# Performance work log

Hardware: AMD Instinct MI355X
Metric: run time of the kernel (lower is better)

Reference implementation:

```python
import jax, jax.numpy as jnp
import numpy as np

EPS = 1e-5
N_NODES = 50000


def batchnorm(x, gamma, beta):
    # training-mode BatchNorm1d: batch mean, biased variance
    mean = jnp.mean(x, axis=0)
    var = jnp.mean(jnp.square(x - mean), axis=0)
    return (x - mean) * jax.lax.rsqrt(var + EPS) * gamma + beta


def setup_inputs() -> dict:
    key = jax.random.key(0)
    ks = jax.random.split(key, 8)
    N, E, D_IN, D_H, D_OUT = N_NODES, 800000, 128, 128, 128
    feat = jax.random.normal(ks[0], (N, D_IN), dtype=jnp.float32)
    w = jax.random.uniform(ks[1], (E,), dtype=jnp.float32)
    # xavier_uniform with relu gain for Q and W
    gain = float(np.sqrt(2.0))
    bq = gain * np.sqrt(6.0 / (D_IN + D_H))
    bw = gain * np.sqrt(6.0 / (D_IN + D_H + D_OUT))
    Q_w = jax.random.uniform(ks[2], (D_H, D_IN), minval=-bq, maxval=bq, dtype=jnp.float32)
    W_w = jax.random.uniform(ks[3], (D_OUT, D_IN + D_H), minval=-bw, maxval=bw, dtype=jnp.float32)
    Q_b = jnp.zeros((D_H,), jnp.float32)
    W_b = jnp.zeros((D_OUT,), jnp.float32)
    gamma2 = jnp.ones((D_OUT,), jnp.float32)
    beta2 = jnp.zeros((D_OUT,), jnp.float32)
    src = jax.random.randint(ks[4], (E,), 0, N, dtype=jnp.int32)
    dst = jax.random.randint(ks[5], (E,), 0, N, dtype=jnp.int32)
    return {"feat": feat, "w": w, "Q_w": Q_w, "Q_b": Q_b, "W_w": W_w,
            "W_b": W_b, "gamma2": gamma2, "beta2": beta2, "src": src, "dst": dst}


def reference(feat, w, Q_w, Q_b, W_w, W_b, gamma2, beta2, src, dst):
    N = feat.shape[0]
    # h = dropout(bnorm_two(relu(Q(feat))))  (dropout=0 -> identity; source reuses bnorm_two)
    h = batchnorm(jax.nn.relu(feat @ Q_w.T + Q_b), gamma2, beta2)  # [N, H]
    # weighted neighbor mean: sum_e w_e * h[src_e] scattered to dst, / sum_e w_e
    num = jax.ops.segment_sum(w[:, None] * h[src], dst, num_segments=N)  # [N, H]
    den = jax.ops.segment_sum(w, dst, num_segments=N)  # [N]
    has_msg = den[:, None] != 0
    agg = jnp.where(has_msg, num / jnp.where(has_msg, den[:, None], 1.0), h)
    rst = jnp.concatenate([feat, agg], axis=1) @ W_w.T + W_b  # [N, OUT]
    rst = batchnorm(jax.nn.relu(rst), gamma2, beta2)
    denom = jnp.linalg.norm(rst, axis=1, keepdims=True)
    return rst / jnp.where(denom == 0, 1.0, denom)
```

## Files before the change

kernel.cpp:

```cpp
#include <hip/hip_runtime.h>
#include <stdint.h>


#define BN_EPS 1e-5f
#define NSLOT 32

typedef __attribute__((ext_vector_type(8))) short bf16x8;
typedef __attribute__((ext_vector_type(4))) float f32x4;

static __device__ __forceinline__ unsigned short f2bf(float f) {
    uint32_t u = __builtin_bit_cast(uint32_t, f);
    u += 0x7fffu + ((u >> 16) & 1u);
    return (unsigned short)(u >> 16);
}
static __device__ __forceinline__ float bf_lo(uint32_t u) {
    return __builtin_bit_cast(float, u << 16);
}
static __device__ __forceinline__ float bf_hi(uint32_t u) {
    return __builtin_bit_cast(float, u & 0xffff0000u);
}

static __device__ __forceinline__ void cast_blk(
    const float* __restrict__ src, unsigned short* __restrict__ dst,
    int n, int blk)
{
    int i = (blk * 256 + threadIdx.x) * 4;
    if (i + 3 < n) {
        float4 v = *(const float4*)(src + i);
        ushort4 o;
        o.x = f2bf(v.x); o.y = f2bf(v.y); o.z = f2bf(v.z); o.w = f2bf(v.w);
        *(ushort4*)(dst + i) = o;
    } else {
        for (int j = i; j < n; ++j) dst[j] = f2bf(src[j]);
    }
}

static __device__ __forceinline__ void scan_ccnt(
    const int* __restrict__ ccnt, int* excl_out, int* v_out, int* w0s)
{
    const int t = threadIdx.x;
    int v = 0, incl = 0;
    if (t < 128) {
        v = ccnt[t];
        incl = v;
        const int lane = t & 63;
#pragma unroll
        for (int o = 1; o < 64; o <<= 1) {
            int u = __shfl_up(incl, o, 64);
            if (lane >= o) incl += u;
        }
        if (t == 63) *w0s = incl;
    }
    __syncthreads();
    int excl = 0;
    if (t < 128) excl = incl - v + ((t >> 6) ? *w0s : 0);
    *excl_out = excl;
    *v_out = v;
}

__global__ __launch_bounds__(256) void k_pre(
    const float* __restrict__ feat, unsigned short* __restrict__ featb, int nf,
    const int* __restrict__ dst, int* __restrict__ ccnt, int E, int CB, int HB,
    const float* __restrict__ Qw, unsigned short* __restrict__ Qwb,
    const float* __restrict__ Ww, unsigned short* __restrict__ Wwb,
    int* __restrict__ offs, int N)
{
    int b = (int)blockIdx.x;
    if (b < CB) {
        if (b == 0 && threadIdx.x == 0) offs[N] = E;
        cast_blk(feat, featb, nf, b);
        return;
    }
    b -= CB;
    if (b >= HB) {
        b -= HB;
        if (b < 16) cast_blk(Qw, Qwb, 128 * 128, b);
        else        cast_blk(Ww, Wwb, 128 * 256, b - 16);
        return;
    }
    __shared__ int hcnt[128];
    const int tid = threadIdx.x;
    if (tid < 128) hcnt[tid] = 0;
    __syncthreads();
    const int base_e = b * 2048;
#pragma unroll
    for (int j = 0; j < 8; ++j) {
        int e = base_e + j * 256 + tid;
        if (e < E) atomicAdd(&hcnt[dst[e] >> 9], 1);
    }
    __syncthreads();
    if (tid < 128 && hcnt[tid] > 0) atomicAdd(&ccnt[tid], hcnt[tid]);
}

template<int K, bool OUT_BF16>
static __device__ __forceinline__ void gemm_body(
    int bid,
    const unsigned short* __restrict__ A_lo,
    const unsigned short* __restrict__ A_hi,
    const unsigned short* __restrict__ Bb,
    const float* __restrict__ bias,
    void* __restrict__ Yv,
    double* __restrict__ sum, double* __restrict__ sumsq, int N)
{
    constexpr int SA = 72;
    __shared__ unsigned short As[64 * SA];
    __shared__ unsigned short Bs[128 * SA];
    __shared__ float bsum_s[128], bsq_s[128];

    const int tid  = threadIdx.x;
    const int lane = tid & 63;
    const int wv   = tid >> 6;
    const int wr   = wv >> 1;
    const int wc   = wv & 1;
    const int m15  = lane & 15;
    const int quad = lane >> 4;
    const int r0   = bid * 64;

    if (tid < 128) { bsum_s[tid] = 0.f; bsq_s[tid] = 0.f; }

    f32x4 acc[2][4];
#pragma unroll
    for (int rt = 0; rt < 2; ++rt)
#pragma unroll
        for (int ct = 0; ct < 4; ++ct)
            acc[rt][ct] = (f32x4){0.f, 0.f, 0.f, 0.f};

    for (int kc = 0; kc < K; kc += 64) {
        const unsigned short* Ap = (kc < 128) ? A_lo : A_hi;
        const int koff = kc & 127;
#pragma unroll
        for (int i = 0; i < 2; ++i) {
            int idx = i * 256 + tid;
            int row = idx >> 3, seg = idx & 7;
            int gr  = r0 + row; if (gr >= N) gr = N - 1;
            uint4 v = *(const uint4*)(Ap + (size_t)gr * 128 + koff + seg * 8);
            *(uint4*)(As + row * SA + seg * 8) = v;
        }
#pragma unroll
        for (int i = 0; i < 4; ++i) {
            int idx = i * 256 + tid;
            int row = idx >> 3, seg = idx & 7;
            uint4 v = *(const uint4*)(Bb + (size_t)row * K + kc + seg * 8);
            *(uint4*)(Bs + row * SA + seg * 8) = v;
        }
        __syncthreads();

#pragma unroll
        for (int ks = 0; ks < 64; ks += 32) {
            bf16x8 af[2], bfr[4];
#pragma unroll
            for (int rt = 0; rt < 2; ++rt)
                af[rt] = *(const bf16x8*)(As + (wr * 32 + rt * 16 + m15) * SA + ks + quad * 8);
#pragma unroll
            for (int ct = 0; ct < 4; ++ct)
                bfr[ct] = *(const bf16x8*)(Bs + (wc * 64 + ct * 16 + m15) * SA + ks + quad * 8);
#pragma unroll
            for (int rt = 0; rt < 2; ++rt)
#pragma unroll
                for (int ct = 0; ct < 4; ++ct)
                    acc[rt][ct] = __builtin_amdgcn_mfma_f32_16x16x32_bf16(
                        af[rt], bfr[ct], acc[rt][ct], 0, 0, 0);
        }
        __syncthreads();
    }

#pragma unroll
    for (int ct = 0; ct < 4; ++ct) {
        int col = wc * 64 + ct * 16 + m15;
        float bz = bias[col];
        float s = 0.f, q = 0.f;
#pragma unroll
        for (int rt = 0; rt < 2; ++rt) {
#pragma unroll
            for (int reg = 0; reg < 4; ++reg) {
                int row = r0 + wr * 32 + rt * 16 + quad * 4 + reg;
                float vv = fmaxf(acc[rt][ct][reg] + bz, 0.f);
                if (row < N) {
                    if constexpr (OUT_BF16)
                        ((unsigned short*)Yv)[(size_t)row * 128 + col] = f2bf(vv);
                    else
                        ((float*)Yv)[(size_t)row * 128 + col] = vv;
                } else {
                    vv = 0.f;
                }
                s += vv; q = fmaf(vv, vv, q);
            }
        }
        s += __shfl_xor(s, 16, 64); s += __shfl_xor(s, 32, 64);
        q += __shfl_xor(q, 16, 64); q += __shfl_xor(q, 32, 64);
        if (quad == 0) {
            atomicAdd(&bsum_s[col], s);
            atomicAdd(&bsq_s[col], q);
        }
    }
    __syncthreads();
    if (tid < 128) {
        const int slot = (bid & (NSLOT - 1)) * 128;
        atomicAdd(&sum[slot + tid],   (double)bsum_s[tid]);
        atomicAdd(&sumsq[slot + tid], (double)bsq_s[tid]);
    }
}

static __device__ __forceinline__ void bn_coef_body(
    int t, const double* __restrict__ sum, const double* __restrict__ sumsq,
    const float* __restrict__ gamma, const float* __restrict__ beta,
    float* __restrict__ a, float* __restrict__ b, double invN)
{
    double ms = 0.0, qs = 0.0;
#pragma unroll
    for (int s = 0; s < NSLOT; ++s) {
        ms += sum[s * 128 + t];
        qs += sumsq[s * 128 + t];
    }
    float mean = (float)(ms * invN);
    float var  = (float)(qs * invN) - mean * mean;
    float sc = rsqrtf(var + BN_EPS) * gamma[t];
    a[t] = sc;
    b[t] = fmaf(-mean, sc, beta[t]);
}

__global__ __launch_bounds__(128) void bn_coef(
    const double* __restrict__ sum, const double* __restrict__ sumsq,
    const float* __restrict__ gamma, const float* __restrict__ beta,
    float* __restrict__ a, float* __restrict__ b, double invN)
{
    bn_coef_body(threadIdx.x, sum, sumsq, gamma, beta, a, b, invN);
}

static __device__ __forceinline__ void bin_body(
    int bid,
    const int* __restrict__ src, const int* __restrict__ dst,
    const float* __restrict__ w,
    const int* __restrict__ ccnt, int* __restrict__ gofs,
    int4* __restrict__ tmp, int E)
{
    __shared__ int hcnt[128];
    __shared__ int hbase[128];
    __shared__ int w0s;
    const int tid = threadIdx.x;
    if (tid < 128) hcnt[tid] = 0;
    __syncthreads();

    int d8[8], s8[8], slot8[8];
    float w8[8];
#pragma unroll
    for (int j = 0; j < 8; ++j) {
        int e = bid * 2048 + j * 256 + tid;
        if (e < E) {
            d8[j] = dst[e]; s8[j] = src[e]; w8[j] = w[e];
            slot8[j] = atomicAdd(&hcnt[d8[j] >> 9], 1);
        } else d8[j] = -1;
    }
    __syncthreads();
    int excl, vcnt;
    scan_ccnt(ccnt, &excl, &vcnt, &w0s);
    if (tid < 128 && hcnt[tid] > 0)
        hbase[tid] = excl + atomicAdd(&gofs[tid], hcnt[tid]);
    __syncthreads();
#pragma unroll
    for (int j = 0; j < 8; ++j) {
        if (d8[j] >= 0) {
            int pos = hbase[d8[j] >> 9] + slot8[j];
            tmp[pos] = make_int4(s8[j], __float_as_int(w8[j]), d8[j], 0);
        }
    }
}

__global__ __launch_bounds__(256) void k_bin_gemm(
    const int* __restrict__ src, const int* __restrict__ dst,
    const float* __restrict__ w,
    const int* __restrict__ ccnt, int* __restrict__ gofs,
    int4* __restrict__ tmp, int E, int HB,
    const unsigned short* __restrict__ featb,
    const unsigned short* __restrict__ Qwb, const float* __restrict__ Qb,
    unsigned short* __restrict__ y1b,
    double* __restrict__ sum, double* __restrict__ sumsq, int N)
{
    if ((int)blockIdx.x < HB)
        bin_body(blockIdx.x, src, dst, w, ccnt, gofs, tmp, E);
    else
        gemm_body<128, true>(blockIdx.x - HB, featb, featb, Qwb, Qb, y1b,
                             sum, sumsq, N);
}

static __device__ __forceinline__ void refine_body(
    int b,
    const int4* __restrict__ tmp, const int* __restrict__ ccnt,
    int* __restrict__ offs, int2* __restrict__ epack, int N)
{
    __shared__ int hist[512];
    __shared__ int wpre[4];
    __shared__ int w0s;
    __shared__ int sbounds[2];
    const int d0   = b << 9;
    const int dlim = min(512, N - d0);
    const int tid  = threadIdx.x;
    const int lane = tid & 63, wv = tid >> 6;

    hist[tid] = 0; hist[tid + 256] = 0;
    __syncthreads();
    int excl, vcnt;
    scan_ccnt(ccnt, &excl, &vcnt, &w0s);
    if (tid == b) { sbounds[0] = excl; sbounds[1] = excl + vcnt; }
    __syncthreads();
    const int start = sbounds[0];
    const int end   = sbounds[1];

    for (int p = start + tid; p < end; p += 256)
        atomicAdd(&hist[tmp[p].z - d0], 1);
    __syncthreads();

    int v0 = hist[2 * tid], v1 = hist[2 * tid + 1];
    int s = v0 + v1;
    int incl = s;
#pragma unroll
    for (int o = 1; o < 64; o <<= 1) {
        int t = __shfl_up(incl, o, 64);
        if (lane >= o) incl += t;
    }
    if (lane == 63) wpre[wv] = incl;
    __syncthreads();
    if (tid == 0) {
        int r = 0;
#pragma unroll
        for (int i = 0; i < 4; ++i) { int t = wpre[i]; wpre[i] = r; r += t; }
    }
    __syncthreads();
    int e0 = start + wpre[wv] + incl - s;
    if (2 * tid < dlim)     offs[d0 + 2 * tid]     = e0;
    if (2 * tid + 1 < dlim) offs[d0 + 2 * tid + 1] = e0 + v0;
    hist[2 * tid]     = e0;
    hist[2 * tid + 1] = e0 + v0;
    __syncthreads();

    for (int p = start + tid; p < end; p += 256) {
        int4 rec = tmp[p];
        int pos = atomicAdd(&hist[rec.z - d0], 1);
        epack[pos] = make_int2(rec.x, rec.y);
    }
}

__global__ __launch_bounds__(256) void k_bnref(
    const double* __restrict__ sum, const double* __restrict__ sumsq,
    const float* __restrict__ gamma, const float* __restrict__ beta,
    float* __restrict__ a, float* __restrict__ b, double invN,
    const int4* __restrict__ tmp, const int* __restrict__ ccnt,
    int* __restrict__ offs, int2* __restrict__ epack, int N)
{
    if (blockIdx.x == 0) {
        if (threadIdx.x < 128)
            bn_coef_body(threadIdx.x, sum, sumsq, gamma, beta, a, b, invN);
        return;
    }
    refine_body((int)blockIdx.x - 1, tmp, ccnt, offs, epack, N);
}

__global__ __launch_bounds__(256) void gather_agg(
    const unsigned short* __restrict__ y1b,
    const int* __restrict__ offs, const int2* __restrict__ epack,
    const float* __restrict__ a, const float* __restrict__ b,
    unsigned short* __restrict__ aggb, int N)
{
    const int r    = (int)((blockIdx.x * 256u + threadIdx.x) >> 6);
    const int lane = threadIdx.x & 63;
    const int li   = lane & 31;
    const int hf   = lane >> 5;
    if (r >= N) return;
    int p = offs[r];
    const int end = offs[r + 1];
    const int c = 4 * li;
    float ac0 = 0.f, ac1 = 0.f, ac2 = 0.f, ac3 = 0.f, den = 0.f;
    for (; p + 7 < end; p += 8) {
        int2 e0 = epack[p + hf];
        int2 e1 = epack[p + 2 + hf];
        int2 e2 = epack[p + 4 + hf];
        int2 e3 = epack[p + 6 + hf];
        uint2 u0 = *(const uint2*)(y1b + (size_t)e0.x * 128 + c);
        uint2 u1 = *(const uint2*)(y1b + (size_t)e1.x * 128 + c);
        uint2 u2 = *(const uint2*)(y1b + (size_t)e2.x * 128 + c);
        uint2 u3 = *(const uint2*)(y1b + (size_t)e3.x * 128 + c);
        float w0 = __int_as_float(e0.y), w1 = __int_as_float(e1.y);
        float w2 = __int_as_float(e2.y), w3 = __int_as_float(e3.y);
        ac0 = fmaf(w0, bf_lo(u0.x), ac0); ac1 = fmaf(w0, bf_hi(u0.x), ac1);
        ac2 = fmaf(w0, bf_lo(u0.y), ac2); ac3 = fmaf(w0, bf_hi(u0.y), ac3);
        ac0 = fmaf(w1, bf_lo(u1.x), ac0); ac1 = fmaf(w1, bf_hi(u1.x), ac1);
        ac2 = fmaf(w1, bf_lo(u1.y), ac2); ac3 = fmaf(w1, bf_hi(u1.y), ac3);
        ac0 = fmaf(w2, bf_lo(u2.x), ac0); ac1 = fmaf(w2, bf_hi(u2.x), ac1);
        ac2 = fmaf(w2, bf_lo(u2.y), ac2); ac3 = fmaf(w2, bf_hi(u2.y), ac3);
        ac0 = fmaf(w3, bf_lo(u3.x), ac0); ac1 = fmaf(w3, bf_hi(u3.x), ac1);
        ac2 = fmaf(w3, bf_lo(u3.y), ac2); ac3 = fmaf(w3, bf_hi(u3.y), ac3);
        den += (w0 + w1) + (w2 + w3);
    }
    for (; p + 3 < end; p += 4) {
        int2 ea = epack[p + hf];
        int2 eb = epack[p + 2 + hf];
        uint2 ua = *(const uint2*)(y1b + (size_t)ea.x * 128 + c);
        uint2 ub = *(const uint2*)(y1b + (size_t)eb.x * 128 + c);
        float wa = __int_as_float(ea.y), wb = __int_as_float(eb.y);
        ac0 = fmaf(wa, bf_lo(ua.x), ac0); ac1 = fmaf(wa, bf_hi(ua.x), ac1);
        ac2 = fmaf(wa, bf_lo(ua.y), ac2); ac3 = fmaf(wa, bf_hi(ua.y), ac3);
        ac0 = fmaf(wb, bf_lo(ub.x), ac0); ac1 = fmaf(wb, bf_hi(ub.x), ac1);
        ac2 = fmaf(wb, bf_lo(ub.y), ac2); ac3 = fmaf(wb, bf_hi(ub.y), ac3);
        den += wa + wb;
    }
    for (; p + 1 < end; p += 2) {
        int2 ea = epack[p + hf];
        uint2 ua = *(const uint2*)(y1b + (size_t)ea.x * 128 + c);
        float wa = __int_as_float(ea.y);
        ac0 = fmaf(wa, bf_lo(ua.x), ac0); ac1 = fmaf(wa, bf_hi(ua.x), ac1);
        ac2 = fmaf(wa, bf_lo(ua.y), ac2); ac3 = fmaf(wa, bf_hi(ua.y), ac3);
        den += wa;
    }
    if (p < end && hf == 0) {
        int2 ea = epack[p];
        uint2 ua = *(const uint2*)(y1b + (size_t)ea.x * 128 + c);
        float wa = __int_as_float(ea.y);
        ac0 = fmaf(wa, bf_lo(ua.x), ac0); ac1 = fmaf(wa, bf_hi(ua.x), ac1);
        ac2 = fmaf(wa, bf_lo(ua.y), ac2); ac3 = fmaf(wa, bf_hi(ua.y), ac3);
        den += wa;
    }
    ac0 += __shfl_xor(ac0, 32, 64);
    ac1 += __shfl_xor(ac1, 32, 64);
    ac2 += __shfl_xor(ac2, 32, 64);
    ac3 += __shfl_xor(ac3, 32, 64);
    den += __shfl_xor(den, 32, 64);
    if (hf) return;
    float4 av = *(const float4*)(a + c);
    float4 bv = *(const float4*)(b + c);
    float m0, m1, m2, m3;
    if (den != 0.f) {
        float inv = 1.f / den;
        m0 = ac0 * inv; m1 = ac1 * inv; m2 = ac2 * inv; m3 = ac3 * inv;
    } else {
        uint2 u = *(const uint2*)(y1b + (size_t)r * 128 + c);
        m0 = bf_lo(u.x); m1 = bf_hi(u.x); m2 = bf_lo(u.y); m3 = bf_hi(u.y);
    }
    ushort4 o;
    o.x = f2bf(fmaf(av.x, m0, bv.x));
    o.y = f2bf(fmaf(av.y, m1, bv.y));
    o.z = f2bf(fmaf(av.z, m2, bv.z));
    o.w = f2bf(fmaf(av.w, m3, bv.w));
    *(ushort4*)(aggb + (size_t)r * 128 + c) = o;
}

__global__ __launch_bounds__(256) void gemm_bn2(
    const unsigned short* __restrict__ A_lo,
    const unsigned short* __restrict__ A_hi,
    const unsigned short* __restrict__ Bb,
    const float* __restrict__ bias,
    float* __restrict__ Y,
    double* __restrict__ sum, double* __restrict__ sumsq, int N)
{
    gemm_body<256, false>(blockIdx.x, A_lo, A_hi, Bb, bias, Y, sum, sumsq, N);
}

__global__ __launch_bounds__(256) void finalize(
    const float* __restrict__ Y2,
    const float* __restrict__ a, const float* __restrict__ b,
    float* __restrict__ out, int N)
{
    __shared__ float sa[128], sb[128];
    const int t = threadIdx.x;
    if (t < 128) { sa[t] = a[t]; sb[t] = b[t]; }
    __syncthreads();
    const int row  = (int)((blockIdx.x * 256u + t) >> 6);
    const int lane = t & 63;
    if (row >= N) return;
    const size_t base = (size_t)row * 128;
    float v0 = fmaf(sa[lane],      Y2[base + lane],      sb[lane]);
    float v1 = fmaf(sa[lane + 64], Y2[base + lane + 64], sb[lane + 64]);
    float ss = fmaf(v0, v0, v1 * v1);
#pragma unroll
    for (int o = 32; o; o >>= 1) ss += __shfl_xor(ss, o, 64);
    float nrm = sqrtf(ss);
    float inv = (nrm == 0.f) ? 1.f : 1.f / nrm;
    out[base + lane]      = v0 * inv;
    out[base + lane + 64] = v1 * inv;
}

extern "C" void kernel_launch(void* const* d_in, const int* in_sizes, int n_in,
                              void* d_out, int out_size, void* d_ws, size_t ws_size,
                              hipStream_t stream)
{
    const float* feat   = (const float*)d_in[0];
    const float* w      = (const float*)d_in[1];
    const float* Q_w    = (const float*)d_in[2];
    const float* Q_b    = (const float*)d_in[3];
    const float* W_w    = (const float*)d_in[4];
    const float* W_b    = (const float*)d_in[5];
    const float* gamma2 = (const float*)d_in[6];
    const float* beta2  = (const float*)d_in[7];
    const int*   src    = (const int*)d_in[8];
    const int*   dst    = (const int*)d_in[9];

    const int N = in_sizes[0] / 128;
    const int E = in_sizes[1];

    float*          y2    = (float*)d_ws;
    unsigned short* featb = (unsigned short*)(y2 + (size_t)N * 128);
    unsigned short* aggb  = featb + (size_t)N * 128;
    unsigned short* y1b   = aggb + (size_t)N * 128;
    int4*  tmp    = (int4*)(y1b + (size_t)N * 128);
    int2*  epack  = (int2*)(tmp + E);
    int*   offs   = (int*)(epack + E);
    float* coefs  = (float*)(offs + N + 1);
    float* a1 = coefs, *b1 = coefs + 128, *a2 = coefs + 256, *b2 = coefs + 384;
    uintptr_t qp = ((uintptr_t)(coefs + 512) + 15) & ~(uintptr_t)15;
    unsigned short* Qwb = (unsigned short*)qp;
    unsigned short* Wwb = Qwb + 128 * 128;
    uintptr_t sp = ((uintptr_t)(Wwb + 128 * 256) + 15) & ~(uintptr_t)15;
    double* stats = (double*)sp;
    double* sum1   = stats;
    double* sumsq1 = stats + NSLOT * 128;
    double* sum2   = stats + 2 * NSLOT * 128;
    double* sumsq2 = stats + 3 * NSLOT * 128;
    int*   ccnt   = (int*)(stats + 4 * NSLOT * 128);
    int*   gofs   = ccnt + 128;

    hipMemsetAsync(stats, 0,
                   4 * NSLOT * 128 * sizeof(double) + 256 * sizeof(int),
                   stream);

    const double invN = 1.0 / (double)N;
    const int GB = (N + 63) / 64;
    const int NB = (N + 511) >> 9;
    const int CB = (N * 128 / 4 + 255) / 256;
    const int HB = (E + 2047) / 2048;
    const int QB = 16;
    const int WB = 32;

    k_pre<<<CB + HB + QB + WB, 256, 0, stream>>>(
        feat, featb, N * 128, dst, ccnt, E, CB, HB,
        Q_w, Qwb, W_w, Wwb, offs, N);

    k_bin_gemm<<<HB + GB, 256, 0, stream>>>(
        src, dst, w, ccnt, gofs, tmp, E, HB,
        featb, Qwb, Q_b, y1b, sum1, sumsq1, N);

    k_bnref<<<NB + 1, 256, 0, stream>>>(
        sum1, sumsq1, gamma2, beta2, a1, b1, invN,
        tmp, ccnt, offs, epack, N);

    gather_agg<<<(N * 64 + 255) / 256, 256, 0, stream>>>(
        y1b, offs, epack, a1, b1, aggb, N);

    gemm_bn2<<<GB, 256, 0, stream>>>(
        featb, aggb, Wwb, W_b, y2, sum2, sumsq2, N);

    bn_coef<<<1, 128, 0, stream>>>(sum2, sumsq2, gamma2, beta2, a2, b2, invN);
    finalize<<<(N * 64 + 255) / 256, 256, 0, stream>>>(
        y2, a2, b2, (float*)d_out, N);
}
```

Baseline: 225.8 us.

## Give second GEMM its own 128x128 tiled MFMA kernel with K-chunked LDS staging

Replaces the shared gemm_body call in gemm_bn2 with a dedicated kernel that computes 128 rows per block. Each of the four waves owns a 64x64 subtile and accumulates in 16 MFMA 16x16x32 bf16 accumulators. The 256-wide K is staged through padded LDS in 64-column chunks, taken from the feat half or the agg half. This halves the grid size and increases per-block reuse of the weight tile, aiming to cut redundant B loads and launch overhead. The trade-off is more registers and a larger LDS footprint, so occupancy may drop, and there are fewer blocks to spread across the CUs.

```diff
diff --git a/kernel.cpp b/kernel.cpp
--- a/kernel.cpp
+++ b/kernel.cpp
@@ -451,7 +451,101 @@
     float* __restrict__ Y,
     double* __restrict__ sum, double* __restrict__ sumsq, int N)
 {
-    gemm_body<256, false>(blockIdx.x, A_lo, A_hi, Bb, bias, Y, sum, sumsq, N);
+    constexpr int SA = 72;
+    constexpr int K = 256;
+    __shared__ unsigned short As[128 * SA];
+    __shared__ unsigned short Bs[128 * SA];
+    __shared__ float bsum_s[128], bsq_s[128];
+
+    const int tid  = threadIdx.x;
+    const int lane = tid & 63;
+    const int wv   = tid >> 6;
+    const int wr   = wv >> 1;
+    const int wc   = wv & 1;
+    const int m15  = lane & 15;
+    const int quad = lane >> 4;
+    const int r0   = (int)blockIdx.x * 128;
+
+    if (tid < 128) { bsum_s[tid] = 0.f; bsq_s[tid] = 0.f; }
+
+    f32x4 acc[4][4];
+#pragma unroll
+    for (int rt = 0; rt < 4; ++rt)
+#pragma unroll
+        for (int ct = 0; ct < 4; ++ct)
+            acc[rt][ct] = (f32x4){0.f, 0.f, 0.f, 0.f};
+
+    for (int kc = 0; kc < K; kc += 64) {
+        const unsigned short* Ap = (kc < 128) ? A_lo : A_hi;
+        const int koff = kc & 127;
+#pragma unroll
+        for (int i = 0; i < 4; ++i) {
+            int idx = i * 256 + tid;
+            int row = idx >> 3, seg = idx & 7;
+            int gr  = r0 + row; if (gr >= N) gr = N - 1;
+            uint4 v = *(const uint4*)(Ap + (size_t)gr * 128 + koff + seg * 8);
+            *(uint4*)(As + row * SA + seg * 8) = v;
+        }
+#pragma unroll
+        for (int i = 0; i < 4; ++i) {
+            int idx = i * 256 + tid;
+            int row = idx >> 3, seg = idx & 7;
+            uint4 v = *(const uint4*)(Bb + (size_t)row * K + kc + seg * 8);
+            *(uint4*)(Bs + row * SA + seg * 8) = v;
+        }
+        __syncthreads();
+
+#pragma unroll
+        for (int ks = 0; ks < 64; ks += 32) {
+            bf16x8 af[4], bfr[4];
+#pragma unroll
+            for (int rt = 0; rt < 4; ++rt)
+                af[rt] = *(const bf16x8*)(As + (wr * 64 + rt * 16 + m15) * SA + ks + quad * 8);
+#pragma unroll
+            for (int ct = 0; ct < 4; ++ct)
+                bfr[ct] = *(const bf16x8*)(Bs + (wc * 64 + ct * 16 + m15) * SA + ks + quad * 8);
+#pragma unroll
+            for (int rt = 0; rt < 4; ++rt)
+#pragma unroll
+                for (int ct = 0; ct < 4; ++ct)
+                    acc[rt][ct] = __builtin_amdgcn_mfma_f32_16x16x32_bf16(
+                        af[rt], bfr[ct], acc[rt][ct], 0, 0, 0);
+        }
+        __syncthreads();
+    }
+
+#pragma unroll
+    for (int ct = 0; ct < 4; ++ct) {
+        int col = wc * 64 + ct * 16 + m15;
+        float bz = bias[col];
+        float s = 0.f, q = 0.f;
+#pragma unroll
+        for (int rt = 0; rt < 4; ++rt) {
+#pragma unroll
+            for (int reg = 0; reg < 4; ++reg) {
+                int row = r0 + wr * 64 + rt * 16 + quad * 4 + reg;
+                float vv = fmaxf(acc[rt][ct][reg] + bz, 0.f);
+                if (row < N) {
+                    Y[(size_t)row * 128 + col] = vv;
+                } else {
+                    vv = 0.f;
+                }
+                s += vv; q = fmaf(vv, vv, q);
+            }
+        }
+        s += __shfl_xor(s, 16, 64); s += __shfl_xor(s, 32, 64);
+        q += __shfl_xor(q, 16, 64); q += __shfl_xor(q, 32, 64);
+        if (quad == 0) {
+            atomicAdd(&bsum_s[col], s);
+            atomicAdd(&bsq_s[col], q);
+        }
+    }
+    __syncthreads();
+    if (tid < 128) {
+        const int slot = ((int)blockIdx.x & (NSLOT - 1)) * 128;
+        atomicAdd(&sum[slot + tid],   (double)bsum_s[tid]);
+        atomicAdd(&sumsq[slot + tid], (double)bsq_s[tid]);
+    }
 }
 
 __global__ __launch_bounds__(256) void finalize(
@@ -522,7 +616,8 @@
                    stream);
 
     const double invN = 1.0 / (double)N;
-    const int GB = (N + 63) / 64;
+    const int GB  = (N + 63) / 64;
+    const int GB2 = (N + 127) / 128;
     const int NB = (N + 511) >> 9;
     const int CB = (N * 128 / 4 + 255) / 256;
     const int HB = (E + 2047) / 2048;
@@ -544,7 +639,7 @@
     gather_agg<<<(N * 64 + 255) / 256, 256, 0, stream>>>(
         y1b, offs, epack, a1, b1, aggb, N);
 
-    gemm_bn2<<<GB, 256, 0, stream>>>(
+    gemm_bn2<<<GB2, 256, 0, stream>>>(
         featb, aggb, Wwb, W_b, y2, sum2, sumsq2, N);
 
     bn_coef<<<1, 128, 0, stream>>>(sum2, sumsq2, gamma2, beta2, a2, b2, invN);
```

New measurement: 223.4 us. About the same (-1.1%).
